# Performance work log

Measured on AMD Instinct MI355X. Metric: run time of the kernel, lower is better.

## Reference

```python
import jax, jax.numpy as jnp
import numpy as np

B, C, H, W = 8, 256, 48, 48
EPS = 1e-5  # BatchNorm2d default eps


def setup_inputs() -> dict:
    key = jax.random.key(0)
    ks = jax.random.split(key, 8)
    return {
        "Q_feat_s": jax.random.normal(ks[0], (B, C, H, W), dtype=jnp.float32),
        "KV_feat_s": jax.random.normal(ks[1], (B, C, H, W), dtype=jnp.float32),
        "Wq": jax.random.normal(ks[2], (C, C), dtype=jnp.float32) * 0.02,
        "Wk": jax.random.normal(ks[3], (C, C), dtype=jnp.float32) * 0.02,
        "Wv": jax.random.normal(ks[4], (C, C), dtype=jnp.float32) * 0.02,
        "Wz": jax.random.normal(ks[5], (C, C), dtype=jnp.float32) * 0.02,
        "bn_gamma": jnp.ones((C,), dtype=jnp.float32),
        "bn_beta": jnp.zeros((C,), dtype=jnp.float32),
        "bn_mean": jax.random.normal(ks[6], (C,), dtype=jnp.float32) * 0.1,
        "bn_var": jax.random.uniform(ks[7], (C,), dtype=jnp.float32, minval=0.5, maxval=1.5),
    }


def reference(Q_feat_s, KV_feat_s, Wq, Wk, Wv, Wz, bn_gamma, bn_beta, bn_mean, bn_var):
    b, c, h, w = Q_feat_s.shape
    n = h * w
    # 1x1 convs == channel-mixing matmuls
    Q = jnp.einsum('oc,bchw->bohw', Wq, Q_feat_s).reshape(b, c, n)      # [B,C,N]
    K = jnp.einsum('oc,bchw->bohw', Wk, KV_feat_s).reshape(b, c, n)     # [B,C,N]
    V = jnp.einsum('oc,bchw->bohw', Wv, KV_feat_s).reshape(b, c, n)     # [B,C,N]
    # attn = (Q^T K)/N then @ V^T; linear (no softmax) so reassociate: Q^T (K V^T)/N
    KV = jnp.einsum('bcn,bdn->bcd', K, V) / n                           # [B,C,C]
    QKV = jnp.einsum('bcn,bcd->bdn', Q, KV)                             # [B,C,N]
    x = QKV.reshape(b, c, h, w)
    # W_z 1x1 conv + BatchNorm2d (inference / running stats)
    z = jnp.einsum('oc,bchw->bohw', Wz, x)
    inv = bn_gamma / jnp.sqrt(bn_var + EPS)
    z = z * inv[None, :, None, None] + (bn_beta - bn_mean * inv)[None, :, None, None]
    return z + Q_feat_s
```

## Files before the change

### kernel.cpp

```cpp
#include <hip/hip_runtime.h>

#define Bv 8
#define Cc 256
#define Nn 2304
#define EPS 1e-5f

typedef float f32x4 __attribute__((ext_vector_type(4)));
typedef __bf16 bf16x8 __attribute__((ext_vector_type(8)));

static __device__ __forceinline__ f32x4 mfma16(bf16x8 a, bf16x8 b, f32x4 c) {
    return __builtin_amdgcn_mfma_f32_16x16x32_bf16(a, b, c, 0, 0, 0);
}

static __device__ __forceinline__ bf16x8 load_cvt8(const float* __restrict__ p) {
    float4 a = *(const float4*)p;
    float4 b = *(const float4*)(p + 4);
    bf16x8 r;
    r[0] = (__bf16)a.x; r[1] = (__bf16)a.y; r[2] = (__bf16)a.z; r[3] = (__bf16)a.w;
    r[4] = (__bf16)b.x; r[5] = (__bf16)b.y; r[6] = (__bf16)b.z; r[7] = (__bf16)b.w;
    return r;
}

__global__ __launch_bounds__(256) void k_lr(
    const float* __restrict__ Wq, const float* __restrict__ Wk,
    const float* __restrict__ Wv, const float* __restrict__ Wz,
    const float* __restrict__ gamma, const float* __restrict__ var_,
    unsigned short* __restrict__ Lb_us, unsigned short* __restrict__ Rtb_us) {
    __shared__ float bufA[4096];
    __shared__ float bufB[4096];
    __bf16* Lb  = (__bf16*)Lb_us;
    __bf16* Rtb = (__bf16*)Rtb_us;
    int blk = blockIdx.x, tid = threadIdx.x;
    bool isL = (blk < 256);
    int t = isL ? blk : blk - 256;
    int tr = (t >> 4) * 16, tc = (t & 15) * 16;
    if (isL) {
        for (int idx = tid; idx < 4096; idx += 256) {
            int r = idx >> 8, m = idx & 255;
            bufA[idx] = Wz[(tr + r) * 256 + m];
        }
        for (int idx = tid; idx < 4096; idx += 256) {
            int m = idx >> 4, j = idx & 15;
            bufB[idx] = Wv[m * 256 + tc + j];
        }
    } else {
        for (int idx = tid; idx < 4096; idx += 256) {
            int o = idx >> 4, j = idx & 15;
            bufA[idx] = Wq[o * 256 + tr + j];
            bufB[idx] = Wk[o * 256 + tc + j];
        }
    }
    __syncthreads();
    int oo = tid >> 4, cc = tid & 15;
    float sum = 0.f;
    if (isL) {
#pragma unroll 8
        for (int m = 0; m < 256; ++m) sum += bufA[oo * 256 + m] * bufB[m * 16 + cc];
        int o = tr + oo;
        float inv = gamma[o] / sqrtf(var_[o] + EPS);
        Lb[o * 256 + tc + cc] = (__bf16)(inv * sum);
    } else {
#pragma unroll 8
        for (int o = 0; o < 256; ++o) sum += bufA[o * 16 + oo] * bufB[o * 16 + cc];
        Rtb[(tr + oo) * 256 + tc + cc] = (__bf16)sum;
    }
}

__global__ __launch_bounds__(256) void k_transpose(
    const float* __restrict__ Qf, unsigned short* __restrict__ Qft_us) {
    __shared__ float tile[64][65];
    __bf16* Qft = (__bf16*)Qft_us;
    int c0 = blockIdx.x * 64, n0 = blockIdx.y * 64, b = blockIdx.z;
    const float* src = Qf + (size_t)b * Cc * Nn;
    int tid = threadIdx.x;
    for (int idx = tid; idx < 4096; idx += 256) {
        int r = idx >> 6, cl = idx & 63;
        tile[r][cl] = src[(size_t)(c0 + r) * Nn + n0 + cl];
    }
    __syncthreads();
    __bf16* dst = Qft + ((size_t)b * Nn + n0) * 256 + c0;
    for (int idx = tid; idx < 4096; idx += 256) {
        int n = idx >> 6, c = idx & 63;
        dst[(size_t)n * 256 + c] = (__bf16)tile[c][n];
    }
}

__global__ __launch_bounds__(256) void k_syrk(
    const float* __restrict__ KVf, float* __restrict__ S) {
    __shared__ __bf16 As[128][40];
    __shared__ __bf16 Bs[128][40];
    int blk = blockIdx.x;
    int b = blk >> 5;
    int quad = (blk >> 3) & 3;
    int kc = blk & 7;
    int rq = quad >> 1, cq = quad & 1;
    int k0 = kc * 288;
    int tid = threadIdx.x;
    int l = tid & 63, w = tid >> 6;
    int wr = w >> 1, wc = w & 1;
    f32x4 zero = {0.f, 0.f, 0.f, 0.f};
    f32x4 acc[4][4];
#pragma unroll
    for (int i = 0; i < 4; ++i)
#pragma unroll
        for (int j = 0; j < 4; ++j) acc[i][j] = zero;

    const float* Abase = KVf + ((size_t)b * Cc + rq * 128) * Nn + k0;
    const float* Bbase = KVf + ((size_t)b * Cc + cq * 128) * Nn + k0;
    int r2 = tid >> 2, cg = (tid & 3) * 8;
    int lr = l & 15, kofs = (l >> 4) * 8;

    for (int ks = 0; ks < 9; ++ks) {
#pragma unroll
        for (int p = 0; p < 2; ++p) {
            int row = p * 64 + r2;
            *(bf16x8*)&As[row][cg] = load_cvt8(Abase + (size_t)row * Nn + ks * 32 + cg);
            *(bf16x8*)&Bs[row][cg] = load_cvt8(Bbase + (size_t)row * Nn + ks * 32 + cg);
        }
        __syncthreads();
        bf16x8 af[4], bb[4];
#pragma unroll
        for (int i = 0; i < 4; ++i) af[i] = *(const bf16x8*)&As[wr * 64 + i * 16 + lr][kofs];
#pragma unroll
        for (int j = 0; j < 4; ++j) bb[j] = *(const bf16x8*)&Bs[wc * 64 + j * 16 + lr][kofs];
#pragma unroll
        for (int i = 0; i < 4; ++i)
#pragma unroll
            for (int j = 0; j < 4; ++j)
                acc[i][j] = mfma16(af[i], bb[j], acc[i][j]);
        __syncthreads();
    }
    const float scale = 1.0f / (float)Nn;
    float* Sb = S + ((size_t)b << 16);
#pragma unroll
    for (int i = 0; i < 4; ++i) {
        int row0 = rq * 128 + wr * 64 + i * 16 + ((l >> 4) << 2);
#pragma unroll
        for (int j = 0; j < 4; ++j) {
            int col = cq * 128 + wc * 64 + j * 16 + lr;
#pragma unroll
            for (int r = 0; r < 4; ++r)
                atomicAdd(&Sb[(size_t)(row0 + r) * 256 + col], acc[i][j][r] * scale);
        }
    }
}

__global__ __launch_bounds__(256) void k_LS(
    const unsigned short* __restrict__ Lb_us, const float* __restrict__ S,
    unsigned short* __restrict__ Tb_us) {
    const __bf16* Lb = (const __bf16*)Lb_us;
    __bf16* Tb = (__bf16*)Tb_us;
    int blk = blockIdx.x;
    int b = blk >> 4, t = blk & 15;
    int tr = (t >> 2) * 64, tc = (t & 3) * 64;
    int tid = threadIdx.x, l = tid & 63, w = tid >> 6;
    int lr = l & 15, kofs = (l >> 4) * 8;
    const float* Sb = S + ((size_t)b << 16);
    f32x4 zero = {0.f, 0.f, 0.f, 0.f};
    f32x4 acc[4] = {zero, zero, zero, zero};
    int arow = tr + w * 16 + lr;
    for (int kk = 0; kk < 256; kk += 32) {
        bf16x8 af = *(const bf16x8*)&Lb[arow * 256 + kk + kofs];
#pragma unroll
        for (int j = 0; j < 4; ++j) {
            int brow = tc + j * 16 + lr;
            bf16x8 bb = load_cvt8(&Sb[(size_t)brow * 256 + kk + kofs]);
            acc[j] = mfma16(af, bb, acc[j]);
        }
    }
    __bf16* Tbb = Tb + ((size_t)b << 16);
    int row0 = tr + w * 16 + ((l >> 4) << 2);
#pragma unroll
    for (int j = 0; j < 4; ++j) {
        int col = tc + j * 16 + lr;
#pragma unroll
        for (int r = 0; r < 4; ++r)
            Tbb[(size_t)(row0 + r) * 256 + col] = (__bf16)acc[j][r];
    }
}

__global__ __launch_bounds__(256) void k_TR(
    const unsigned short* __restrict__ Tb_us, const unsigned short* __restrict__ Rtb_us,
    unsigned short* __restrict__ Pb_us) {
    const __bf16* Tb = (const __bf16*)Tb_us;
    const __bf16* Rtb = (const __bf16*)Rtb_us;
    __bf16* Pb = (__bf16*)Pb_us;
    int blk = blockIdx.x;
    int b = blk >> 4, t = blk & 15;
    int tr = (t >> 2) * 64, tc = (t & 3) * 64;
    int tid = threadIdx.x, l = tid & 63, w = tid >> 6;
    int lr = l & 15, kofs = (l >> 4) * 8;
    const __bf16* Tbb = Tb + ((size_t)b << 16);
    f32x4 zero = {0.f, 0.f, 0.f, 0.f};
    f32x4 acc[4] = {zero, zero, zero, zero};
    int arow = tr + w * 16 + lr;
    for (int kk = 0; kk < 256; kk += 32) {
        bf16x8 af = *(const bf16x8*)&Tbb[(size_t)arow * 256 + kk + kofs];
#pragma unroll
        for (int j = 0; j < 4; ++j) {
            int brow = tc + j * 16 + lr;
            bf16x8 bb = *(const bf16x8*)&Rtb[(size_t)brow * 256 + kk + kofs];
            acc[j] = mfma16(af, bb, acc[j]);
        }
    }
    __bf16* Pbb = Pb + ((size_t)b << 16);
    int row0 = tr + w * 16 + ((l >> 4) << 2);
#pragma unroll
    for (int j = 0; j < 4; ++j) {
        int col = tc + j * 16 + lr;
#pragma unroll
        for (int r = 0; r < 4; ++r)
            Pbb[(size_t)(row0 + r) * 256 + col] = (__bf16)acc[j][r];
    }
}

__global__ __launch_bounds__(256) void k_out(
    const unsigned short* __restrict__ Pb_us, const unsigned short* __restrict__ Qft_us,
    const float* __restrict__ Qf,
    const float* __restrict__ gamma, const float* __restrict__ beta,
    const float* __restrict__ mean, const float* __restrict__ var_,
    float* __restrict__ out) {
    const __bf16* Pb = (const __bf16*)Pb_us;
    const __bf16* Qft = (const __bf16*)Qft_us;
    int nt = blockIdx.x, oh = blockIdx.y, b = blockIdx.z;
    int tid = threadIdx.x, l = tid & 63, w = tid >> 6;
    int wr = w >> 1, wc = w & 1;
    int lr = l & 15, kofs = (l >> 4) * 8;
    int obase = oh * 128 + wr * 64;
    int nbase = nt * 128 + wc * 64;
    const __bf16* A = Pb + ((size_t)b << 16);
    const __bf16* Bt = Qft + (size_t)b * Nn * 256;
    f32x4 zero = {0.f, 0.f, 0.f, 0.f};
    f32x4 acc[4][4];
#pragma unroll
    for (int i = 0; i < 4; ++i)
#pragma unroll
        for (int j = 0; j < 4; ++j) acc[i][j] = zero;

    for (int kk = 0; kk < 256; kk += 32) {
        bf16x8 af[4], bb[4];
#pragma unroll
        for (int i = 0; i < 4; ++i)
            af[i] = *(const bf16x8*)&A[(size_t)(obase + i * 16 + lr) * 256 + kk + kofs];
#pragma unroll
        for (int j = 0; j < 4; ++j)
            bb[j] = *(const bf16x8*)&Bt[(size_t)(nbase + j * 16 + lr) * 256 + kk + kofs];
#pragma unroll
        for (int i = 0; i < 4; ++i)
#pragma unroll
            for (int j = 0; j < 4; ++j)
                acc[i][j] = mfma16(af[i], bb[j], acc[i][j]);
    }

    const float* Qfb = Qf + (size_t)b * Cc * Nn;
    float* outb = out + (size_t)b * Cc * Nn;
#pragma unroll
    for (int i = 0; i < 4; ++i) {
        int o0 = obase + i * 16 + ((l >> 4) << 2);
#pragma unroll
        for (int r = 0; r < 4; ++r) {
            int o = o0 + r;
            float inv = gamma[o] / sqrtf(var_[o] + EPS);
            float shift = beta[o] - mean[o] * inv;
#pragma unroll
            for (int j = 0; j < 4; ++j) {
                int n = nbase + j * 16 + lr;
                outb[(size_t)o * Nn + n] = acc[i][j][r] + shift + Qfb[(size_t)o * Nn + n];
            }
        }
    }
}

extern "C" void kernel_launch(void* const* d_in, const int* in_sizes, int n_in,
                              void* d_out, int out_size, void* d_ws, size_t ws_size,
                              hipStream_t stream) {
    (void)in_sizes; (void)n_in; (void)out_size; (void)ws_size;
    const float* Qf    = (const float*)d_in[0];
    const float* KVf   = (const float*)d_in[1];
    const float* Wq    = (const float*)d_in[2];
    const float* Wk    = (const float*)d_in[3];
    const float* Wv    = (const float*)d_in[4];
    const float* Wz    = (const float*)d_in[5];
    const float* gamma = (const float*)d_in[6];
    const float* beta  = (const float*)d_in[7];
    const float* mean  = (const float*)d_in[8];
    const float* var_  = (const float*)d_in[9];
    float* out = (float*)d_out;

    char* ws = (char*)d_ws;
    float* S            = (float*)ws;
    unsigned short* Lb  = (unsigned short*)(ws + (2u << 20));
    unsigned short* Rtb = (unsigned short*)(ws + (2u << 20) + (128u << 10));
    unsigned short* Tb  = (unsigned short*)(ws + (2u << 20) + (256u << 10));
    unsigned short* Pb  = (unsigned short*)(ws + (3u << 20) + (256u << 10));
    unsigned short* Qft = (unsigned short*)(ws + (4u << 20) + (256u << 10));

    hipMemsetAsync(S, 0, (size_t)Bv * 256 * 256 * sizeof(float), stream);
    k_lr<<<512, 256, 0, stream>>>(Wq, Wk, Wv, Wz, gamma, var_, Lb, Rtb);
    k_transpose<<<dim3(4, 36, 8), 256, 0, stream>>>(Qf, Qft);
    k_syrk<<<256, 256, 0, stream>>>(KVf, S);
    k_LS<<<128, 256, 0, stream>>>(Lb, S, Tb);
    k_TR<<<128, 256, 0, stream>>>(Tb, Rtb, Pb);
    k_out<<<dim3(18, 2, 8), 256, 0, stream>>>(Pb, Qft, Qf, gamma, beta, mean, var_, out);
}
```

Baseline: 184.7 us.

## Fuse prep kernels, replace atomic syrk with split-K partials, merge LS and TR

Merges the weight-product, Q transpose and KV Gram kernels into one launch dispatched by block index. The Gram matrix now writes two split-K partial buffers with plain stores instead of atomics, so the memset goes away. The two small chained GEMMs are merged into one kernel that keeps the intermediate in shared memory. k_out gets a new grid and warp tiling. This cuts launch count and atomic traffic, but the merged small-GEMM stage runs only 32 blocks and the Gram stage has less parallelism per block.

Result: slower. 237.4 us (+28.5%).

```diff
diff --git a/kernel.cpp b/kernel.cpp
--- a/kernel.cpp
+++ b/kernel.cpp
@@ -21,196 +21,191 @@
     return r;
 }
 
-__global__ __launch_bounds__(256) void k_lr(
+static __device__ __forceinline__ bf16x8 load_add_cvt8(const float* __restrict__ p0,
+                                                       const float* __restrict__ p1) {
+    float4 a0 = *(const float4*)p0;
+    float4 a1 = *(const float4*)(p0 + 4);
+    float4 b0 = *(const float4*)p1;
+    float4 b1 = *(const float4*)(p1 + 4);
+    bf16x8 r;
+    r[0] = (__bf16)(a0.x + b0.x); r[1] = (__bf16)(a0.y + b0.y);
+    r[2] = (__bf16)(a0.z + b0.z); r[3] = (__bf16)(a0.w + b0.w);
+    r[4] = (__bf16)(a1.x + b1.x); r[5] = (__bf16)(a1.y + b1.y);
+    r[6] = (__bf16)(a1.z + b1.z); r[7] = (__bf16)(a1.w + b1.w);
+    return r;
+}
+
+__global__ __launch_bounds__(256) void k_fused1(
+    const float* __restrict__ Qf, const float* __restrict__ KVf,
     const float* __restrict__ Wq, const float* __restrict__ Wk,
     const float* __restrict__ Wv, const float* __restrict__ Wz,
     const float* __restrict__ gamma, const float* __restrict__ var_,
-    unsigned short* __restrict__ Lb_us, unsigned short* __restrict__ Rtb_us) {
-    __shared__ float bufA[4096];
-    __shared__ float bufB[4096];
-    __bf16* Lb  = (__bf16*)Lb_us;
-    __bf16* Rtb = (__bf16*)Rtb_us;
+    unsigned short* __restrict__ Lb_us, unsigned short* __restrict__ Rtb_us,
+    unsigned short* __restrict__ Qft_us, float* __restrict__ Spart) {
+    __shared__ __align__(16) char smem[32768];
     int blk = blockIdx.x, tid = threadIdx.x;
-    bool isL = (blk < 256);
-    int t = isL ? blk : blk - 256;
-    int tr = (t >> 4) * 16, tc = (t & 15) * 16;
-    if (isL) {
+
+    if (blk < 512) {
+        float* bufA = (float*)smem;
+        float* bufB = bufA + 4096;
+        __bf16* Lb  = (__bf16*)Lb_us;
+        __bf16* Rtb = (__bf16*)Rtb_us;
+        bool isL = (blk < 256);
+        int t = isL ? blk : blk - 256;
+        int tr = (t >> 4) * 16, tc = (t & 15) * 16;
+        if (isL) {
+            for (int idx = tid; idx < 4096; idx += 256) {
+                int r = idx >> 8, m = idx & 255;
+                bufA[idx] = Wz[(tr + r) * 256 + m];
+            }
+            for (int idx = tid; idx < 4096; idx += 256) {
+                int m = idx >> 4, j = idx & 15;
+                bufB[idx] = Wv[m * 256 + tc + j];
+            }
+        } else {
+            for (int idx = tid; idx < 4096; idx += 256) {
+                int o = idx >> 4, j = idx & 15;
+                bufA[idx] = Wq[o * 256 + tr + j];
+                bufB[idx] = Wk[o * 256 + tc + j];
+            }
+        }
+        __syncthreads();
+        int oo = tid >> 4, cc = tid & 15;
+        float sum = 0.f;
+        if (isL) {
+#pragma unroll 8
+            for (int m = 0; m < 256; ++m) sum += bufA[oo * 256 + m] * bufB[m * 16 + cc];
+            int o = tr + oo;
+            float inv = gamma[o] / sqrtf(var_[o] + EPS);
+            Lb[o * 256 + tc + cc] = (__bf16)(inv * sum * (1.0f / (float)Nn));
+        } else {
+#pragma unroll 8
+            for (int o = 0; o < 256; ++o) sum += bufA[o * 16 + oo] * bufB[o * 16 + cc];
+            Rtb[(tr + oo) * 256 + tc + cc] = (__bf16)sum;
+        }
+    } else if (blk < 1664) {
+        float (*tile)[65] = (float (*)[65])smem;
+        __bf16* Qft = (__bf16*)Qft_us;
+        int t = blk - 512;
+        int c0 = (t & 3) * 64;
+        int u = t >> 2;
+        int n0 = (u % 36) * 64;
+        int b = u / 36;
+        const float* src = Qf + (size_t)b * Cc * Nn;
         for (int idx = tid; idx < 4096; idx += 256) {
-            int r = idx >> 8, m = idx & 255;
-            bufA[idx] = Wz[(tr + r) * 256 + m];
-        }
+            int r = idx >> 6, cl = idx & 63;
+            tile[r][cl] = src[(size_t)(c0 + r) * Nn + n0 + cl];
+        }
+        __syncthreads();
+        __bf16* dst = Qft + ((size_t)b * Nn + n0) * 256 + c0;
         for (int idx = tid; idx < 4096; idx += 256) {
-            int m = idx >> 4, j = idx & 15;
-            bufB[idx] = Wv[m * 256 + tc + j];
+            int n = idx >> 6, c = idx & 63;
+            dst[(size_t)n * 256 + c] = (__bf16)tile[c][n];
         }
     } else {
-        for (int idx = tid; idx < 4096; idx += 256) {
-            int o = idx >> 4, j = idx & 15;
-            bufA[idx] = Wq[o * 256 + tr + j];
-            bufB[idx] = Wk[o * 256 + tc + j];
-        }
-    }
-    __syncthreads();
-    int oo = tid >> 4, cc = tid & 15;
-    float sum = 0.f;
-    if (isL) {
-#pragma unroll 8
-        for (int m = 0; m < 256; ++m) sum += bufA[oo * 256 + m] * bufB[m * 16 + cc];
-        int o = tr + oo;
-        float inv = gamma[o] / sqrtf(var_[o] + EPS);
-        Lb[o * 256 + tc + cc] = (__bf16)(inv * sum);
-    } else {
-#pragma unroll 8
-        for (int o = 0; o < 256; ++o) sum += bufA[o * 16 + oo] * bufB[o * 16 + cc];
-        Rtb[(tr + oo) * 256 + tc + cc] = (__bf16)sum;
-    }
-}
-
-__global__ __launch_bounds__(256) void k_transpose(
-    const float* __restrict__ Qf, unsigned short* __restrict__ Qft_us) {
-    __shared__ float tile[64][65];
-    __bf16* Qft = (__bf16*)Qft_us;
-    int c0 = blockIdx.x * 64, n0 = blockIdx.y * 64, b = blockIdx.z;
-    const float* src = Qf + (size_t)b * Cc * Nn;
-    int tid = threadIdx.x;
-    for (int idx = tid; idx < 4096; idx += 256) {
-        int r = idx >> 6, cl = idx & 63;
-        tile[r][cl] = src[(size_t)(c0 + r) * Nn + n0 + cl];
-    }
-    __syncthreads();
-    __bf16* dst = Qft + ((size_t)b * Nn + n0) * 256 + c0;
-    for (int idx = tid; idx < 4096; idx += 256) {
-        int n = idx >> 6, c = idx & 63;
-        dst[(size_t)n * 256 + c] = (__bf16)tile[c][n];
-    }
-}
-
-__global__ __launch_bounds__(256) void k_syrk(
-    const float* __restrict__ KVf, float* __restrict__ S) {
-    __shared__ __bf16 As[128][40];
-    __shared__ __bf16 Bs[128][40];
-    int blk = blockIdx.x;
-    int b = blk >> 5;
-    int quad = (blk >> 3) & 3;
-    int kc = blk & 7;
-    int rq = quad >> 1, cq = quad & 1;
-    int k0 = kc * 288;
-    int tid = threadIdx.x;
-    int l = tid & 63, w = tid >> 6;
-    int wr = w >> 1, wc = w & 1;
-    f32x4 zero = {0.f, 0.f, 0.f, 0.f};
-    f32x4 acc[4][4];
-#pragma unroll
-    for (int i = 0; i < 4; ++i)
-#pragma unroll
-        for (int j = 0; j < 4; ++j) acc[i][j] = zero;
-
-    const float* Abase = KVf + ((size_t)b * Cc + rq * 128) * Nn + k0;
-    const float* Bbase = KVf + ((size_t)b * Cc + cq * 128) * Nn + k0;
-    int r2 = tid >> 2, cg = (tid & 3) * 8;
-    int lr = l & 15, kofs = (l >> 4) * 8;
-
-    for (int ks = 0; ks < 9; ++ks) {
-#pragma unroll
-        for (int p = 0; p < 2; ++p) {
-            int row = p * 64 + r2;
-            *(bf16x8*)&As[row][cg] = load_cvt8(Abase + (size_t)row * Nn + ks * 32 + cg);
-            *(bf16x8*)&Bs[row][cg] = load_cvt8(Bbase + (size_t)row * Nn + ks * 32 + cg);
-        }
-        __syncthreads();
-        bf16x8 af[4], bb[4];
-#pragma unroll
-        for (int i = 0; i < 4; ++i) af[i] = *(const bf16x8*)&As[wr * 64 + i * 16 + lr][kofs];
-#pragma unroll
-        for (int j = 0; j < 4; ++j) bb[j] = *(const bf16x8*)&Bs[wc * 64 + j * 16 + lr][kofs];
-#pragma unroll
-        for (int i = 0; i < 4; ++i)
-#pragma unroll
-            for (int j = 0; j < 4; ++j)
-                acc[i][j] = mfma16(af[i], bb[j], acc[i][j]);
-        __syncthreads();
-    }
-    const float scale = 1.0f / (float)Nn;
-    float* Sb = S + ((size_t)b << 16);
-#pragma unroll
-    for (int i = 0; i < 4; ++i) {
-        int row0 = rq * 128 + wr * 64 + i * 16 + ((l >> 4) << 2);
+        __bf16 (*As)[40] = (__bf16 (*)[40])smem;
+        __bf16 (*Bs)[40] = (__bf16 (*)[40])(smem + 5120);
+        int sblk = blk - 1664;
+        int b = sblk & 7;
+        int tt = (sblk >> 3) & 15;
+        int kc = sblk >> 7;
+        int tr = (tt >> 2) * 64, tc = (tt & 3) * 64;
+        int k0 = kc * 1152;
+        int l = tid & 63, w = tid >> 6;
+        int lr = l & 15, kofs = (l >> 4) * 8;
+        int r2 = tid >> 2, cg = (tid & 3) * 8;
+        const float* Abase = KVf + ((size_t)b * Cc + tr) * Nn + k0;
+        const float* Bbase = KVf + ((size_t)b * Cc + tc) * Nn + k0;
+        f32x4 zero = {0.f, 0.f, 0.f, 0.f};
+        f32x4 acc[4] = {zero, zero, zero, zero};
+        for (int ks = 0; ks < 36; ++ks) {
+            *(bf16x8*)&As[r2][cg] = load_cvt8(Abase + (size_t)r2 * Nn + ks * 32 + cg);
+            *(bf16x8*)&Bs[r2][cg] = load_cvt8(Bbase + (size_t)r2 * Nn + ks * 32 + cg);
+            __syncthreads();
+            bf16x8 af = *(const bf16x8*)&As[w * 16 + lr][kofs];
+#pragma unroll
+            for (int j = 0; j < 4; ++j) {
+                bf16x8 bb = *(const bf16x8*)&Bs[j * 16 + lr][kofs];
+                acc[j] = mfma16(af, bb, acc[j]);
+            }
+            __syncthreads();
+        }
+        float* Sp = Spart + ((size_t)kc * Bv + b) * 65536;
+        int row0 = tr + w * 16 + ((l >> 4) << 2);
 #pragma unroll
         for (int j = 0; j < 4; ++j) {
-            int col = cq * 128 + wc * 64 + j * 16 + lr;
+            int col = tc + j * 16 + lr;
 #pragma unroll
             for (int r = 0; r < 4; ++r)
-                atomicAdd(&Sb[(size_t)(row0 + r) * 256 + col], acc[i][j][r] * scale);
-        }
-    }
-}
-
-__global__ __launch_bounds__(256) void k_LS(
-    const unsigned short* __restrict__ Lb_us, const float* __restrict__ S,
-    unsigned short* __restrict__ Tb_us) {
+                Sp[(size_t)(row0 + r) * 256 + col] = acc[j][r];
+        }
+    }
+}
+
+__global__ __launch_bounds__(256) void k_LSR(
+    const unsigned short* __restrict__ Lb_us, const float* __restrict__ Spart,
+    const unsigned short* __restrict__ Rtb_us, unsigned short* __restrict__ Pb_us) {
+    __shared__ __bf16 Ts[64][264];
     const __bf16* Lb = (const __bf16*)Lb_us;
-    __bf16* Tb = (__bf16*)Tb_us;
-    int blk = blockIdx.x;
-    int b = blk >> 4, t = blk & 15;
-    int tr = (t >> 2) * 64, tc = (t & 3) * 64;
-    int tid = threadIdx.x, l = tid & 63, w = tid >> 6;
-    int lr = l & 15, kofs = (l >> 4) * 8;
-    const float* Sb = S + ((size_t)b << 16);
-    f32x4 zero = {0.f, 0.f, 0.f, 0.f};
-    f32x4 acc[4] = {zero, zero, zero, zero};
-    int arow = tr + w * 16 + lr;
-    for (int kk = 0; kk < 256; kk += 32) {
-        bf16x8 af = *(const bf16x8*)&Lb[arow * 256 + kk + kofs];
-#pragma unroll
-        for (int j = 0; j < 4; ++j) {
-            int brow = tc + j * 16 + lr;
-            bf16x8 bb = load_cvt8(&Sb[(size_t)brow * 256 + kk + kofs]);
-            acc[j] = mfma16(af, bb, acc[j]);
-        }
-    }
-    __bf16* Tbb = Tb + ((size_t)b << 16);
-    int row0 = tr + w * 16 + ((l >> 4) << 2);
-#pragma unroll
-    for (int j = 0; j < 4; ++j) {
-        int col = tc + j * 16 + lr;
-#pragma unroll
-        for (int r = 0; r < 4; ++r)
-            Tbb[(size_t)(row0 + r) * 256 + col] = (__bf16)acc[j][r];
-    }
-}
-
-__global__ __launch_bounds__(256) void k_TR(
-    const unsigned short* __restrict__ Tb_us, const unsigned short* __restrict__ Rtb_us,
-    unsigned short* __restrict__ Pb_us) {
-    const __bf16* Tb = (const __bf16*)Tb_us;
     const __bf16* Rtb = (const __bf16*)Rtb_us;
     __bf16* Pb = (__bf16*)Pb_us;
     int blk = blockIdx.x;
-    int b = blk >> 4, t = blk & 15;
-    int tr = (t >> 2) * 64, tc = (t & 3) * 64;
+    int b = blk & 7, rt = blk >> 3;
+    int r0 = rt * 64;
     int tid = threadIdx.x, l = tid & 63, w = tid >> 6;
     int lr = l & 15, kofs = (l >> 4) * 8;
-    const __bf16* Tbb = Tb + ((size_t)b << 16);
+    const float* S0 = Spart + (size_t)b * 65536;
+    const float* S1 = Spart + (size_t)(Bv + b) * 65536;
     f32x4 zero = {0.f, 0.f, 0.f, 0.f};
-    f32x4 acc[4] = {zero, zero, zero, zero};
-    int arow = tr + w * 16 + lr;
-    for (int kk = 0; kk < 256; kk += 32) {
-        bf16x8 af = *(const bf16x8*)&Tbb[(size_t)arow * 256 + kk + kofs];
-#pragma unroll
-        for (int j = 0; j < 4; ++j) {
-            int brow = tc + j * 16 + lr;
-            bf16x8 bb = *(const bf16x8*)&Rtb[(size_t)brow * 256 + kk + kofs];
-            acc[j] = mfma16(af, bb, acc[j]);
-        }
-    }
-    __bf16* Pbb = Pb + ((size_t)b << 16);
-    int row0 = tr + w * 16 + ((l >> 4) << 2);
-#pragma unroll
-    for (int j = 0; j < 4; ++j) {
-        int col = tc + j * 16 + lr;
-#pragma unroll
-        for (int r = 0; r < 4; ++r)
-            Pbb[(size_t)(row0 + r) * 256 + col] = (__bf16)acc[j][r];
+
+    {
+        f32x4 acc[16];
+#pragma unroll
+        for (int j = 0; j < 16; ++j) acc[j] = zero;
+        int arow = r0 + w * 16 + lr;
+        for (int kk = 0; kk < 256; kk += 32) {
+            bf16x8 af = *(const bf16x8*)&Lb[arow * 256 + kk + kofs];
+#pragma unroll
+            for (int j = 0; j < 16; ++j) {
+                int brow = j * 16 + lr;
+                bf16x8 bb = load_add_cvt8(&S0[(size_t)brow * 256 + kk + kofs],
+                                          &S1[(size_t)brow * 256 + kk + kofs]);
+                acc[j] = mfma16(af, bb, acc[j]);
+            }
+        }
+        int rloc = w * 16 + ((l >> 4) << 2);
+#pragma unroll
+        for (int j = 0; j < 16; ++j) {
+            int col = j * 16 + lr;
+#pragma unroll
+            for (int r = 0; r < 4; ++r)
+                Ts[rloc + r][col] = (__bf16)acc[j][r];
+        }
+    }
+    __syncthreads();
+
+    {
+        f32x4 acc[16];
+#pragma unroll
+        for (int j = 0; j < 16; ++j) acc[j] = zero;
+        for (int kk = 0; kk < 256; kk += 32) {
+            bf16x8 af = *(const bf16x8*)&Ts[w * 16 + lr][kk + kofs];
+#pragma unroll
+            for (int j = 0; j < 16; ++j) {
+                int brow = j * 16 + lr;
+                bf16x8 bb = *(const bf16x8*)&Rtb[brow * 256 + kk + kofs];
+                acc[j] = mfma16(af, bb, acc[j]);
+            }
+        }
+        __bf16* Pbb = Pb + ((size_t)b << 16);
+        int row0 = r0 + w * 16 + ((l >> 4) << 2);
+#pragma unroll
+        for (int j = 0; j < 16; ++j) {
+            int col = j * 16 + lr;
+#pragma unroll
+            for (int r = 0; r < 4; ++r)
+                Pbb[(size_t)(row0 + r) * 256 + col] = (__bf16)acc[j][r];
+        }
     }
 }
 
@@ -222,12 +217,12 @@
     float* __restrict__ out) {
     const __bf16* Pb = (const __bf16*)Pb_us;
     const __bf16* Qft = (const __bf16*)Qft_us;
-    int nt = blockIdx.x, oh = blockIdx.y, b = blockIdx.z;
+    int bid = blockIdx.x;
+    int b = bid & 7, nt = bid >> 3;
     int tid = threadIdx.x, l = tid & 63, w = tid >> 6;
-    int wr = w >> 1, wc = w & 1;
     int lr = l & 15, kofs = (l >> 4) * 8;
-    int obase = oh * 128 + wr * 64;
-    int nbase = nt * 128 + wc * 64;
+    int obase = w * 64;
+    int nbase = nt * 64;
     const __bf16* A = Pb + ((size_t)b << 16);
     const __bf16* Bt = Qft + (size_t)b * Nn * 256;
     f32x4 zero = {0.f, 0.f, 0.f, 0.f};
@@ -288,18 +283,14 @@
     float* out = (float*)d_out;
 
     char* ws = (char*)d_ws;
-    float* S            = (float*)ws;
-    unsigned short* Lb  = (unsigned short*)(ws + (2u << 20));
-    unsigned short* Rtb = (unsigned short*)(ws + (2u << 20) + (128u << 10));
-    unsigned short* Tb  = (unsigned short*)(ws + (2u << 20) + (256u << 10));
-    unsigned short* Pb  = (unsigned short*)(ws + (3u << 20) + (256u << 10));
-    unsigned short* Qft = (unsigned short*)(ws + (4u << 20) + (256u << 10));
-
-    hipMemsetAsync(S, 0, (size_t)Bv * 256 * 256 * sizeof(float), stream);
-    k_lr<<<512, 256, 0, stream>>>(Wq, Wk, Wv, Wz, gamma, var_, Lb, Rtb);
-    k_transpose<<<dim3(4, 36, 8), 256, 0, stream>>>(Qf, Qft);
-    k_syrk<<<256, 256, 0, stream>>>(KVf, S);
-    k_LS<<<128, 256, 0, stream>>>(Lb, S, Tb);
-    k_TR<<<128, 256, 0, stream>>>(Tb, Rtb, Pb);
-    k_out<<<dim3(18, 2, 8), 256, 0, stream>>>(Pb, Qft, Qf, gamma, beta, mean, var_, out);
-}
+    float* Spart        = (float*)ws;
+    unsigned short* Lb  = (unsigned short*)(ws + (4u << 20));
+    unsigned short* Rtb = (unsigned short*)(ws + (4u << 20) + (128u << 10));
+    unsigned short* Pb  = (unsigned short*)(ws + (4u << 20) + (256u << 10));
+    unsigned short* Qft = (unsigned short*)(ws + (5u << 20) + (256u << 10));
+
+    k_fused1<<<1920, 256, 0, stream>>>(Qf, KVf, Wq, Wk, Wv, Wz, gamma, var_,
+                                       Lb, Rtb, Qft, Spart);
+    k_LSR<<<32, 256, 0, stream>>>(Lb, Spart, Rtb, Pb);
+    k_out<<<288, 256, 0, stream>>>(Pb, Qft, Qf, gamma, beta, mean, var_, out);
+}
```
